# Optimization experiments

Measured on AMD Instinct MI355X. Metric: run time of the kernel, lower is better.

The kernel has to match this reference:

```python
import jax, jax.numpy as jnp
import numpy as np

B, T, C, H, D = 2, 2048, 1024, 16, 64

def setup_inputs() -> dict:
    key = jax.random.key(0)
    ks = jax.random.split(key, 5)
    s = 1.0 / np.sqrt(C)
    return {
        "hidden_states": jax.random.normal(ks[0], (B, T, C), jnp.float32),
        "Wq": jax.random.normal(ks[1], (H, C, D), jnp.float32) * s,
        "Wk": jax.random.normal(ks[2], (H, C, D), jnp.float32) * s,
        "Wv": jax.random.normal(ks[3], (H, C, D), jnp.float32) * s,
        "Wo": jax.random.normal(ks[4], (C, C), jnp.float32) * s,
    }

def reference(hidden_states, Wq, Wk, Wv, Wo):
    x = hidden_states  # (B, T, C)
    q = jnp.einsum("btc,hcd->bhtd", x, Wq)
    k = jnp.einsum("btc,hcd->bhtd", x, Wk)
    v = jnp.einsum("btc,hcd->bhtd", x, Wv)
    scale = 1.0 / jnp.sqrt(jnp.asarray(D, x.dtype))
    scores = jnp.einsum("bhtd,bhsd->bhts", q, k) * scale  # (B,H,T,T)
    Tlen = x.shape[1]
    causal = jnp.tril(jnp.ones((Tlen, Tlen), bool))
    scores = jnp.where(causal, scores, jnp.asarray(-jnp.inf, x.dtype))
    probs = jax.nn.softmax(scores, axis=-1)
    heads = jnp.einsum("bhts,bhsd->bhtd", probs, v)  # (B,H,T,D)
    concat = heads.transpose(0, 2, 1, 3).reshape(x.shape[0], Tlen, H * D)  # (B,T,C)
    return jnp.einsum("btc,oc->bto", concat, Wo)  # output projection (dropout=0)
```

## Files before the change

kernel.cpp:

```cpp
#include <hip/hip_runtime.h>
#include <math.h>

#define B_ 2
#define T_ 2048
#define C_ 1024
#define H_ 16
#define D_ 64

typedef short short8 __attribute__((ext_vector_type(8)));
typedef float f32x4 __attribute__((ext_vector_type(4)));

#define LOG2E 1.44269504088896f

__device__ __forceinline__ unsigned short f2bf(float f) {
    unsigned int u = __float_as_uint(f);
    u += 0x7FFFu + ((u >> 16) & 1u);
    return (unsigned short)(u >> 16);
}
__device__ __forceinline__ unsigned short f2bf_fast(float f) {
    return (unsigned short)((__float_as_uint(f) + 0x8000u) >> 16);
}

__global__ __launch_bounds__(256) void prep_cast(
    const float* __restrict__ x, const float* __restrict__ wo,
    unsigned short* __restrict__ xb, unsigned short* __restrict__ wob,
    int nX, int nW)
{
    int i = (blockIdx.x * 256 + threadIdx.x) * 8;
    const float* s;
    unsigned short* d;
    if (i < nX) { s = x + i; d = xb + i; }
    else {
        int j = i - nX;
        if (j >= nW) return;
        s = wo + j; d = wob + j;
    }
    float4 a = *(const float4*)s;
    float4 b = *(const float4*)(s + 4);
    ushort4 o0, o1;
    o0.x = f2bf(a.x); o0.y = f2bf(a.y); o0.z = f2bf(a.z); o0.w = f2bf(a.w);
    o1.x = f2bf(b.x); o1.y = f2bf(b.y); o1.z = f2bf(b.z); o1.w = f2bf(b.w);
    *(ushort4*)d = o0;
    *(ushort4*)(d + 4) = o1;
}

__global__ __launch_bounds__(256) void transpose_w(
    const float* __restrict__ Wq, const float* __restrict__ Wk,
    const float* __restrict__ Wv,
    unsigned short* __restrict__ Wqt, unsigned short* __restrict__ Wkt,
    unsigned short* __restrict__ Wvt)
{
    __shared__ float t[64][65];
    const int c0 = blockIdx.x * 64;
    const int h  = blockIdx.y;
    const int z  = blockIdx.z;
    const float* W = (z == 0) ? Wq : (z == 1) ? Wk : Wv;
    unsigned short* Wt = (z == 0) ? Wqt : (z == 1) ? Wkt : Wvt;
    const int tid = threadIdx.x;
    const int r = tid >> 4, c4 = (tid & 15) * 4;
    #pragma unroll
    for (int p = 0; p < 4; p++) {
        int cl = r + p * 16;
        float4 v = *(const float4*)&W[((size_t)h * C_ + c0 + cl) * D_ + c4];
        t[cl][c4 + 0] = v.x; t[cl][c4 + 1] = v.y;
        t[cl][c4 + 2] = v.z; t[cl][c4 + 3] = v.w;
    }
    __syncthreads();
    #pragma unroll
    for (int p = 0; p < 4; p++) {
        int d = r + p * 16;
        ushort4 o;
        o.x = f2bf(t[c4 + 0][d]); o.y = f2bf(t[c4 + 1][d]);
        o.z = f2bf(t[c4 + 2][d]); o.w = f2bf(t[c4 + 3][d]);
        *(ushort4*)&Wt[((size_t)h * D_ + d) * C_ + c0 + c4] = o;
    }
}

__global__ __launch_bounds__(256) void qkv_big(
    const unsigned short* __restrict__ X,
    const unsigned short* __restrict__ Wall,
    unsigned short* __restrict__ Qo,
    unsigned short* __restrict__ Ko,
    unsigned short* __restrict__ Vt)
{
    __shared__ unsigned short As[128][72];
    __shared__ unsigned short Bs[128][72];

    const int m0 = blockIdx.x * 128;
    const int n0 = blockIdx.y * 128;
    const int z  = n0 >> 10;
    const int tid = threadIdx.x;
    const int w = tid >> 6, lane = tid & 63, quad = lane >> 4, l16 = lane & 15;
    const int wm = w & 1, wn = w >> 1;
    const int lrow = tid >> 3, lcol = (tid & 7) * 8;

    f32x4 acc[4][4] = {};

    short8 ar[4], br[4];
    #pragma unroll
    for (int p = 0; p < 4; p++) {
        int r = lrow + p * 32;
        ar[p] = *(const short8*)&X[(size_t)(m0 + r) * C_ + lcol];
        br[p] = *(const short8*)&Wall[(size_t)(n0 + r) * C_ + lcol];
    }

    for (int k0 = 0; k0 < C_; k0 += 64) {
        __syncthreads();
        #pragma unroll
        for (int p = 0; p < 4; p++) {
            int r = lrow + p * 32;
            *(short8*)&As[r][lcol] = ar[p];
            *(short8*)&Bs[r][lcol] = br[p];
        }
        __syncthreads();
        if (k0 + 64 < C_) {
            #pragma unroll
            for (int p = 0; p < 4; p++) {
                int r = lrow + p * 32;
                ar[p] = *(const short8*)&X[(size_t)(m0 + r) * C_ + k0 + 64 + lcol];
                br[p] = *(const short8*)&Wall[(size_t)(n0 + r) * C_ + k0 + 64 + lcol];
            }
        }
        #pragma unroll
        for (int ks = 0; ks < 2; ks++) {
            short8 af[4], bf[4];
            #pragma unroll
            for (int i = 0; i < 4; i++)
                af[i] = *(const short8*)&As[wm * 64 + i * 16 + l16][ks * 32 + quad * 8];
            #pragma unroll
            for (int j = 0; j < 4; j++)
                bf[j] = *(const short8*)&Bs[wn * 64 + j * 16 + l16][ks * 32 + quad * 8];
            #pragma unroll
            for (int i = 0; i < 4; i++)
                #pragma unroll
                for (int j = 0; j < 4; j++)
                    acc[i][j] = __builtin_amdgcn_mfma_f32_16x16x32_bf16(af[i], bf[j], acc[i][j], 0, 0, 0);
        }
    }

    if (z == 2) {
        #pragma unroll
        for (int j = 0; j < 4; j++) {
            const int n = n0 + wn * 64 + j * 16 + l16;
            const int h = (n >> 6) & 15, d = n & 63;
            #pragma unroll
            for (int i = 0; i < 4; i++) {
                const int m = m0 + wm * 64 + i * 16 + quad * 4;
                const int b = m >> 11, t = m & (T_ - 1);
                ushort4 pk;
                pk.x = f2bf(acc[i][j][0]);
                pk.y = f2bf(acc[i][j][1]);
                pk.z = f2bf(acc[i][j][2]);
                pk.w = f2bf(acc[i][j][3]);
                *(ushort4*)&Vt[(((size_t)b * H_ + h) * D_ + d) * T_ + t] = pk;
            }
        }
    } else {
        const float scale = (z == 0) ? 0.125f * LOG2E : 1.0f;
        unsigned short* O = (z == 0) ? Qo : Ko;
        #pragma unroll
        for (int j = 0; j < 4; j++) {
            const int n = n0 + wn * 64 + j * 16 + l16;
            const int h = (n >> 6) & 15, d = n & 63;
            #pragma unroll
            for (int i = 0; i < 4; i++)
                #pragma unroll
                for (int r = 0; r < 4; r++) {
                    const int m = m0 + wm * 64 + i * 16 + quad * 4 + r;
                    const int b = m >> 11, t = m & (T_ - 1);
                    O[(((size_t)b * H_ + h) * T_ + t) * D_ + d] = f2bf(acc[i][j][r] * scale);
                }
        }
    }
}

__global__ __launch_bounds__(256) void flash_mfma(
    const unsigned short* __restrict__ Q,
    const unsigned short* __restrict__ K,
    const unsigned short* __restrict__ Vt,
    unsigned short* __restrict__ CC)
{
    __shared__ unsigned short kst[64][72];
    __shared__ unsigned short vts[64][72];
    __shared__ unsigned short ps[64][80];

    const int qb = 31 - blockIdx.x;
    const int h = blockIdx.y, b = blockIdx.z;
    const int q0 = qb * 64;
    const int tid = threadIdx.x;
    const int w = tid >> 6, lane = tid & 63, quad = lane >> 4, l16 = lane & 15;
    const int lrow = tid >> 3, lcol = (tid & 7) * 8;
    const size_t hb  = ((size_t)b * H_ + h) * T_;
    const size_t hbD = ((size_t)b * H_ + h) * D_;

    short8 qf[2];
    #pragma unroll
    for (int ks = 0; ks < 2; ks++)
        qf[ks] = *(const short8*)&Q[(hb + q0 + w * 16 + l16) * D_ + ks * 32 + quad * 8];

    float l_part[4] = {0.f, 0.f, 0.f, 0.f};
    f32x4 o[4] = {};

    short8 kreg[2], vreg[2];
    #pragma unroll
    for (int p = 0; p < 2; p++) {
        int r = lrow + p * 32;
        kreg[p] = *(const short8*)&K[(hb + r) * D_ + lcol];
        vreg[p] = *(const short8*)&Vt[(hbD + r) * T_ + lcol];
    }

    for (int kb = 0; kb <= qb; kb++) {
        __syncthreads();
        #pragma unroll
        for (int p = 0; p < 2; p++) {
            int r = lrow + p * 32;
            *(short8*)&kst[r][lcol] = kreg[p];
            *(short8*)&vts[r][lcol] = vreg[p];
        }
        __syncthreads();
        if (kb < qb) {
            const int k0n = (kb + 1) * 64;
            #pragma unroll
            for (int p = 0; p < 2; p++) {
                int r = lrow + p * 32;
                kreg[p] = *(const short8*)&K[(hb + k0n + r) * D_ + lcol];
                vreg[p] = *(const short8*)&Vt[(hbD + r) * T_ + k0n + lcol];
            }
        }

        f32x4 s[4] = {};
        #pragma unroll
        for (int ks = 0; ks < 2; ks++)
            #pragma unroll
            for (int ct = 0; ct < 4; ct++) {
                short8 kf = *(const short8*)&kst[ct * 16 + l16][ks * 32 + quad * 8];
                s[ct] = __builtin_amdgcn_mfma_f32_16x16x32_bf16(qf[ks], kf, s[ct], 0, 0, 0);
            }

        if (kb == qb) {
            #pragma unroll
            for (int ct = 0; ct < 4; ct++)
                #pragma unroll
                for (int r = 0; r < 4; r++) {
                    int qr = w * 16 + quad * 4 + r;
                    int kc = ct * 16 + l16;
                    if (kc > qr) s[ct][r] = -INFINITY;
                }
        }

        #pragma unroll
        for (int ct = 0; ct < 4; ct++)
            #pragma unroll
            for (int r = 0; r < 4; r++) {
                float p = exp2f(s[ct][r]);
                l_part[r] += p;
                ps[w * 16 + quad * 4 + r][ct * 16 + l16] = f2bf_fast(p);
            }

        #pragma unroll
        for (int ks = 0; ks < 2; ks++) {
            short8 pa = *(const short8*)&ps[w * 16 + l16][ks * 32 + quad * 8];
            #pragma unroll
            for (int ct = 0; ct < 4; ct++) {
                short8 vf = *(const short8*)&vts[ct * 16 + l16][ks * 32 + quad * 8];
                o[ct] = __builtin_amdgcn_mfma_f32_16x16x32_bf16(pa, vf, o[ct], 0, 0, 0);
            }
        }
    }

    #pragma unroll
    for (int r = 0; r < 4; r++) {
        float ls = l_part[r];
        ls += __shfl_xor(ls, 1);
        ls += __shfl_xor(ls, 2);
        ls += __shfl_xor(ls, 4);
        ls += __shfl_xor(ls, 8);
        float invl = 1.0f / ls;
        int t = q0 + w * 16 + quad * 4 + r;
        #pragma unroll
        for (int ct = 0; ct < 4; ct++)
            CC[((size_t)b * T_ + t) * C_ + h * D_ + ct * 16 + l16] = f2bf(o[ct][r] * invl);
    }
}

__global__ __launch_bounds__(256) void out_big(
    const unsigned short* __restrict__ X,
    const unsigned short* __restrict__ Wob,
    float* __restrict__ out)
{
    __shared__ unsigned short As[128][72];
    __shared__ unsigned short Bs[128][72];

    const int m0 = blockIdx.x * 128;
    const int n0 = blockIdx.y * 128;
    const int tid = threadIdx.x;
    const int w = tid >> 6, lane = tid & 63, quad = lane >> 4, l16 = lane & 15;
    const int wm = w & 1, wn = w >> 1;
    const int lrow = tid >> 3, lcol = (tid & 7) * 8;

    f32x4 acc[4][4] = {};

    short8 ar[4], br[4];
    #pragma unroll
    for (int p = 0; p < 4; p++) {
        int r = lrow + p * 32;
        ar[p] = *(const short8*)&X[(size_t)(m0 + r) * C_ + lcol];
        br[p] = *(const short8*)&Wob[(size_t)(n0 + r) * C_ + lcol];
    }

    for (int k0 = 0; k0 < C_; k0 += 64) {
        __syncthreads();
        #pragma unroll
        for (int p = 0; p < 4; p++) {
            int r = lrow + p * 32;
            *(short8*)&As[r][lcol] = ar[p];
            *(short8*)&Bs[r][lcol] = br[p];
        }
        __syncthreads();
        if (k0 + 64 < C_) {
            #pragma unroll
            for (int p = 0; p < 4; p++) {
                int r = lrow + p * 32;
                ar[p] = *(const short8*)&X[(size_t)(m0 + r) * C_ + k0 + 64 + lcol];
                br[p] = *(const short8*)&Wob[(size_t)(n0 + r) * C_ + k0 + 64 + lcol];
            }
        }
        #pragma unroll
        for (int ks = 0; ks < 2; ks++) {
            short8 af[4], bf[4];
            #pragma unroll
            for (int i = 0; i < 4; i++)
                af[i] = *(const short8*)&As[wm * 64 + i * 16 + l16][ks * 32 + quad * 8];
            #pragma unroll
            for (int j = 0; j < 4; j++)
                bf[j] = *(const short8*)&Bs[wn * 64 + j * 16 + l16][ks * 32 + quad * 8];
            #pragma unroll
            for (int i = 0; i < 4; i++)
                #pragma unroll
                for (int j = 0; j < 4; j++)
                    acc[i][j] = __builtin_amdgcn_mfma_f32_16x16x32_bf16(af[i], bf[j], acc[i][j], 0, 0, 0);
        }
    }

    #pragma unroll
    for (int i = 0; i < 4; i++)
        #pragma unroll
        for (int j = 0; j < 4; j++)
            #pragma unroll
            for (int r = 0; r < 4; r++)
                out[(size_t)(m0 + wm * 64 + i * 16 + quad * 4 + r) * C_ + n0 + wn * 64 + j * 16 + l16] = acc[i][j][r];
}

extern "C" void kernel_launch(void* const* d_in, const int* in_sizes, int n_in,
                              void* d_out, int out_size, void* d_ws, size_t ws_size,
                              hipStream_t stream) {
    const float* x  = (const float*)d_in[0];
    const float* Wq = (const float*)d_in[1];
    const float* Wk = (const float*)d_in[2];
    const float* Wv = (const float*)d_in[3];
    const float* Wo = (const float*)d_in[4];
    float* out = (float*)d_out;

    const size_t nX = (size_t)B_ * T_ * C_;
    const size_t nW = (size_t)H_ * C_ * D_;
    const size_t nQ = (size_t)B_ * H_ * T_ * D_;
    unsigned short* xb   = (unsigned short*)d_ws;
    unsigned short* Wall = xb + nX;
    unsigned short* Wqt  = Wall;
    unsigned short* Wkt  = Wqt + nW;
    unsigned short* Wvt  = Wkt + nW;
    unsigned short* Wob  = Wvt + nW;
    unsigned short* Qb   = Wob + nW;
    unsigned short* Kb   = Qb + nQ;
    unsigned short* Vtb  = Kb + nQ;
    unsigned short* CCb  = Vtb + nQ;

    prep_cast<<<dim3((unsigned)((nX + nW) / 2048)), 256, 0, stream>>>(
        x, Wo, xb, Wob, (int)nX, (int)nW);
    transpose_w<<<dim3(C_ / 64, H_, 3), 256, 0, stream>>>(Wq, Wk, Wv, Wqt, Wkt, Wvt);
    qkv_big<<<dim3(32, 24), 256, 0, stream>>>(xb, Wall, Qb, Kb, Vtb);
    flash_mfma<<<dim3(32, H_, B_), 256, 0, stream>>>(Qb, Kb, Vtb, CCb);
    out_big<<<dim3(32, 8), 256, 0, stream>>>(CCb, Wob, out);
}
```

Baseline: 204.9 us.

## Pair causal query blocks per workgroup and split KV range across two thread groups

The flash attention kernel now runs 512-thread blocks that each handle two query blocks (qb and 31-qb) in sequence, which evens out the causal workload across blocks. Within each query block, two 256-thread groups process alternating KV tiles in parallel, and their partial outputs and row sums are merged through shared memory at the end. This targets load imbalance from the causal triangle and adds parallelism per query tile. The cost is extra shared memory, extra barriers, and a reduction step per phase.

```diff
diff --git a/kernel.cpp b/kernel.cpp
--- a/kernel.cpp
+++ b/kernel.cpp
@@ -174,112 +174,153 @@
     }
 }
 
-__global__ __launch_bounds__(256) void flash_mfma(
+__global__ __launch_bounds__(512, 4) void flash_mfma(
     const unsigned short* __restrict__ Q,
     const unsigned short* __restrict__ K,
     const unsigned short* __restrict__ Vt,
     unsigned short* __restrict__ CC)
 {
-    __shared__ unsigned short kst[64][72];
-    __shared__ unsigned short vts[64][72];
-    __shared__ unsigned short ps[64][80];
-
-    const int qb = 31 - blockIdx.x;
-    const int h = blockIdx.y, b = blockIdx.z;
-    const int q0 = qb * 64;
+    __shared__ unsigned short kst[2][64][72];
+    __shared__ unsigned short vts[2][64][72];
+    __shared__ unsigned short ps [2][64][72];
+
+    const int pairid = blockIdx.x, h = blockIdx.y, b = blockIdx.z;
     const int tid = threadIdx.x;
-    const int w = tid >> 6, lane = tid & 63, quad = lane >> 4, l16 = lane & 15;
-    const int lrow = tid >> 3, lcol = (tid & 7) * 8;
+    const int g  = tid >> 8;
+    const int t2 = tid & 255;
+    const int w = t2 >> 6, lane = t2 & 63, quad = lane >> 4, l16 = lane & 15;
+    const int lrow = t2 >> 3, lcol = (t2 & 7) * 8;
     const size_t hb  = ((size_t)b * H_ + h) * T_;
     const size_t hbD = ((size_t)b * H_ + h) * D_;
 
-    short8 qf[2];
-    #pragma unroll
-    for (int ks = 0; ks < 2; ks++)
-        qf[ks] = *(const short8*)&Q[(hb + q0 + w * 16 + l16) * D_ + ks * 32 + quad * 8];
-
-    float l_part[4] = {0.f, 0.f, 0.f, 0.f};
-    f32x4 o[4] = {};
-
-    short8 kreg[2], vreg[2];
-    #pragma unroll
-    for (int p = 0; p < 2; p++) {
-        int r = lrow + p * 32;
-        kreg[p] = *(const short8*)&K[(hb + r) * D_ + lcol];
-        vreg[p] = *(const short8*)&Vt[(hbD + r) * T_ + lcol];
-    }
-
-    for (int kb = 0; kb <= qb; kb++) {
-        __syncthreads();
-        #pragma unroll
-        for (int p = 0; p < 2; p++) {
-            int r = lrow + p * 32;
-            *(short8*)&kst[r][lcol] = kreg[p];
-            *(short8*)&vts[r][lcol] = vreg[p];
-        }
-        __syncthreads();
-        if (kb < qb) {
-            const int k0n = (kb + 1) * 64;
+    float* fob = (float*)&kst[0][0][0];
+    float* flb = (float*)&ps[0][0][0];
+
+    for (int phase = 0; phase < 2; phase++) {
+        const int qb = phase ? 31 - pairid : pairid;
+        const int q0 = qb * 64;
+        const int nkb = qb + 1;
+        const int maxit = (nkb + 1) >> 1;
+
+        short8 qf[2];
+        #pragma unroll
+        for (int ks = 0; ks < 2; ks++)
+            qf[ks] = *(const short8*)&Q[(hb + q0 + w * 16 + l16) * D_ + ks * 32 + quad * 8];
+
+        float l_part[4] = {0.f, 0.f, 0.f, 0.f};
+        f32x4 o[4] = {};
+
+        short8 kreg[2], vreg[2];
+        {
+            const int k0 = g * 64;
             #pragma unroll
             for (int p = 0; p < 2; p++) {
                 int r = lrow + p * 32;
-                kreg[p] = *(const short8*)&K[(hb + k0n + r) * D_ + lcol];
-                vreg[p] = *(const short8*)&Vt[(hbD + r) * T_ + k0n + lcol];
-            }
-        }
-
-        f32x4 s[4] = {};
-        #pragma unroll
-        for (int ks = 0; ks < 2; ks++)
-            #pragma unroll
-            for (int ct = 0; ct < 4; ct++) {
-                short8 kf = *(const short8*)&kst[ct * 16 + l16][ks * 32 + quad * 8];
-                s[ct] = __builtin_amdgcn_mfma_f32_16x16x32_bf16(qf[ks], kf, s[ct], 0, 0, 0);
-            }
-
-        if (kb == qb) {
-            #pragma unroll
-            for (int ct = 0; ct < 4; ct++)
-                #pragma unroll
-                for (int r = 0; r < 4; r++) {
-                    int qr = w * 16 + quad * 4 + r;
-                    int kc = ct * 16 + l16;
-                    if (kc > qr) s[ct][r] = -INFINITY;
-                }
-        }
-
-        #pragma unroll
-        for (int ct = 0; ct < 4; ct++)
+                kreg[p] = *(const short8*)&K[(hb + k0 + r) * D_ + lcol];
+                vreg[p] = *(const short8*)&Vt[(hbD + r) * T_ + k0 + lcol];
+            }
+        }
+
+        for (int it = 0; it < maxit; it++) {
+            const int kb = 2 * it + g;
+            const bool act = (kb < nkb);
+            __syncthreads();
+            if (act) {
+                #pragma unroll
+                for (int p = 0; p < 2; p++) {
+                    int r = lrow + p * 32;
+                    *(short8*)&kst[g][r][lcol] = kreg[p];
+                    *(short8*)&vts[g][r][lcol] = vreg[p];
+                }
+            }
+            __syncthreads();
+            if (kb + 2 < nkb) {
+                const int k0n = (kb + 2) * 64;
+                #pragma unroll
+                for (int p = 0; p < 2; p++) {
+                    int r = lrow + p * 32;
+                    kreg[p] = *(const short8*)&K[(hb + k0n + r) * D_ + lcol];
+                    vreg[p] = *(const short8*)&Vt[(hbD + r) * T_ + k0n + lcol];
+                }
+            }
+            if (act) {
+                f32x4 s[4] = {};
+                #pragma unroll
+                for (int ks = 0; ks < 2; ks++)
+                    #pragma unroll
+                    for (int ct = 0; ct < 4; ct++) {
+                        short8 kf = *(const short8*)&kst[g][ct * 16 + l16][ks * 32 + quad * 8];
+                        s[ct] = __builtin_amdgcn_mfma_f32_16x16x32_bf16(qf[ks], kf, s[ct], 0, 0, 0);
+                    }
+
+                if (kb == qb) {
+                    #pragma unroll
+                    for (int ct = 0; ct < 4; ct++)
+                        #pragma unroll
+                        for (int r = 0; r < 4; r++) {
+                            int qr = w * 16 + quad * 4 + r;
+                            int kc = ct * 16 + l16;
+                            if (kc > qr) s[ct][r] = -INFINITY;
+                        }
+                }
+
+                #pragma unroll
+                for (int ct = 0; ct < 4; ct++)
+                    #pragma unroll
+                    for (int r = 0; r < 4; r++) {
+                        float p = exp2f(s[ct][r]);
+                        l_part[r] += p;
+                        ps[g][w * 16 + quad * 4 + r][ct * 16 + l16] = f2bf_fast(p);
+                    }
+
+                #pragma unroll
+                for (int ks = 0; ks < 2; ks++) {
+                    short8 pa = *(const short8*)&ps[g][w * 16 + l16][ks * 32 + quad * 8];
+                    #pragma unroll
+                    for (int ct = 0; ct < 4; ct++) {
+                        short8 vf = *(const short8*)&vts[g][ct * 16 + l16][ks * 32 + quad * 8];
+                        o[ct] = __builtin_amdgcn_mfma_f32_16x16x32_bf16(pa, vf, o[ct], 0, 0, 0);
+                    }
+                }
+            }
+        }
+
+        __syncthreads();
+        if (g == 1) {
             #pragma unroll
             for (int r = 0; r < 4; r++) {
-                float p = exp2f(s[ct][r]);
-                l_part[r] += p;
-                ps[w * 16 + quad * 4 + r][ct * 16 + l16] = f2bf_fast(p);
-            }
-
-        #pragma unroll
-        for (int ks = 0; ks < 2; ks++) {
-            short8 pa = *(const short8*)&ps[w * 16 + l16][ks * 32 + quad * 8];
-            #pragma unroll
-            for (int ct = 0; ct < 4; ct++) {
-                short8 vf = *(const short8*)&vts[ct * 16 + l16][ks * 32 + quad * 8];
-                o[ct] = __builtin_amdgcn_mfma_f32_16x16x32_bf16(pa, vf, o[ct], 0, 0, 0);
-            }
-        }
-    }
-
-    #pragma unroll
-    for (int r = 0; r < 4; r++) {
-        float ls = l_part[r];
-        ls += __shfl_xor(ls, 1);
-        ls += __shfl_xor(ls, 2);
-        ls += __shfl_xor(ls, 4);
-        ls += __shfl_xor(ls, 8);
-        float invl = 1.0f / ls;
-        int t = q0 + w * 16 + quad * 4 + r;
-        #pragma unroll
-        for (int ct = 0; ct < 4; ct++)
-            CC[((size_t)b * T_ + t) * C_ + h * D_ + ct * 16 + l16] = f2bf(o[ct][r] * invl);
+                float ls = l_part[r];
+                ls += __shfl_xor(ls, 1);
+                ls += __shfl_xor(ls, 2);
+                ls += __shfl_xor(ls, 4);
+                ls += __shfl_xor(ls, 8);
+                if (l16 == 0) flb[w * 16 + quad * 4 + r] = ls;
+                #pragma unroll
+                for (int ct = 0; ct < 4; ct++)
+                    fob[(w * 16 + quad * 4 + r) * 68 + ct * 16 + l16] = o[ct][r];
+            }
+        }
+        __syncthreads();
+        if (g == 0) {
+            #pragma unroll
+            for (int r = 0; r < 4; r++) {
+                float ls = l_part[r];
+                ls += __shfl_xor(ls, 1);
+                ls += __shfl_xor(ls, 2);
+                ls += __shfl_xor(ls, 4);
+                ls += __shfl_xor(ls, 8);
+                const int q = w * 16 + quad * 4 + r;
+                ls += flb[q];
+                const float invl = 1.0f / ls;
+                const int t = q0 + q;
+                #pragma unroll
+                for (int ct = 0; ct < 4; ct++) {
+                    float ov = o[ct][r] + fob[q * 68 + ct * 16 + l16];
+                    CC[((size_t)b * T_ + t) * C_ + h * D_ + ct * 16 + l16] = f2bf(ov * invl);
+                }
+            }
+        }
+        __syncthreads();
     }
 }
 
@@ -379,6 +420,6 @@
         x, Wo, xb, Wob, (int)nX, (int)nW);
     transpose_w<<<dim3(C_ / 64, H_, 3), 256, 0, stream>>>(Wq, Wk, Wv, Wqt, Wkt, Wvt);
     qkv_big<<<dim3(32, 24), 256, 0, stream>>>(xb, Wall, Qb, Kb, Vtb);
-    flash_mfma<<<dim3(32, H_, B_), 256, 0, stream>>>(Qb, Kb, Vtb, CCb);
+    flash_mfma<<<dim3(16, H_, B_), 512, 0, stream>>>(Qb, Kb, Vtb, CCb);
     out_big<<<dim3(32, 8), 256, 0, stream>>>(CCb, Wob, out);
 }
```

Result: faster. 181.8 us (-11.3%).
